# Performance work log

Hardware: AMD Instinct MI355X
Metric: run time of the kernel (lower is better)

Reference implementation:

```python
import jax, jax.numpy as jnp
import numpy as np

SIGMA = 0.248
PRNUM = 6
P = 7.5
K = 3.0
ALPHA = 2.5


def _gauss_kernel():
    # 5x5 normalized Gaussian, replicated per channel for depthwise conv [O=3,I=1,5,5]
    x = jnp.arange(-2, 3, dtype=jnp.float32)
    x2, y2 = jnp.meshgrid(x, x, indexing='xy')
    k = jnp.exp(-(x2 ** 2 + y2 ** 2) / (2.0 * SIGMA ** 2))
    k = k / jnp.sum(k)
    return jnp.broadcast_to(k[None, None], (3, 1, 5, 5))


def _dwconv(x, k):
    # x: [3,H,W]; depthwise 5x5 conv, padding=2 (matches F.conv2d(..., padding=2, groups=3))
    return jax.lax.conv_general_dilated(
        x[None], k, window_strides=(1, 1), padding=[(2, 2), (2, 2)],
        feature_group_count=3, dimension_numbers=('NCHW', 'OIHW', 'NCHW'))[0]


def _down2(x):
    # torch bilinear align_corners=False at exact scale 0.5 == 2x2 average pooling
    c, h, w = x.shape
    return x.reshape(c, h // 2, 2, w // 2, 2).mean(axis=(2, 4))


def _up(x, hw):
    # torch bilinear align_corners=False upsample (half-pixel centers) == jax linear resize
    return jax.image.resize(x, (x.shape[0], hw[0], hw[1]), method='linear')


def _foveate(img, fixs):
    C, H, W = img.shape
    k = _gauss_kernel()
    # build Gaussian pyramid
    G = img
    pyr = [G]
    for _ in range(1, PRNUM):
        G = _down2(_dwconv(G, k))
        pyr.append(G)
    # re-expand each level back to full res (interpolate then blur at each step)
    As = [pyr[0]]
    for i in range(1, PRNUM):
        cur = pyr[i]
        for j in range(i):
            hw = (cur.shape[1] * 2, cur.shape[2] * 2) if j < i - 1 else (H, W)
            cur = _dwconv(_up(cur, hw), k)
        As.append(cur)
    As = jnp.stack(As)  # [prNum, 3, H, W]

    # radial eccentricity map (min distance over fixations)
    x = jnp.arange(W, dtype=jnp.float32)
    y = jnp.arange(H, dtype=jnp.float32)
    x2d, y2d = jnp.meshgrid(x, y, indexing='xy')  # each [H, W]
    d = jnp.sqrt((x2d[None] - fixs[:, 0, None, None]) ** 2 +
                 (y2d[None] - fixs[:, 1, None, None]) ** 2) / P
    theta = jnp.min(d, axis=0)
    R = ALPHA / (theta + ALPHA)

    Ts = [jnp.exp(-((2.0 ** (i - 3)) * R / SIGMA) ** 2 * K) for i in range(1, PRNUM)]
    Ts.append(jnp.zeros_like(R))

    om = np.minimum(np.sqrt(np.log(2.0) / K) / (2.0 ** np.arange(-2, 3)) * SIGMA, 1.0)
    omega = np.concatenate([om, [0.0]]).astype(np.float32)  # [prNum]

    layer_ind = jnp.zeros_like(R)
    for i in range(1, PRNUM):
        ind = (R >= omega[i]) & (R <= omega[i - 1])
        layer_ind = jnp.where(ind, jnp.float32(i), layer_ind)

    Bs = [(0.5 - Ts[i]) / (Ts[i - 1] - Ts[i] + 1e-5) for i in range(1, PRNUM)]

    Ms = []
    for i in range(PRNUM):
        base = jnp.ones_like(R) if i == 0 else 1.0 - Bs[i - 1]
        M = jnp.where(layer_ind == i, base, jnp.float32(0.0))
        if i < PRNUM - 1:
            M = jnp.where(layer_ind == i + 1, Bs[i], M)
        Ms.append(M)
    Ms = jnp.stack(Ms)  # [prNum, H, W]

    # blend: sum_p Ms[p] * As[p, c]
    im_fov = jnp.einsum('phw,pchw->chw', Ms, As)
    return im_fov


def setup_inputs() -> dict:
    key = jax.random.key(0)
    k1, k2 = jax.random.split(key)
    img = jax.random.uniform(k1, (3, 2048, 2048), dtype=jnp.float32) * 255.0
    fixs = jax.random.uniform(k2, (4, 2), dtype=jnp.float32) * 2048.0
    return {'img': img, 'fixs': fixs}


def reference(img, fixs):
    return _foveate(img, fixs)
```

## Files before the change

### kernel.cpp

```cpp
#include <hip/hip_runtime.h>
#include <math.h>

#define HW2048 (2048ull*2048ull)
typedef float f4 __attribute__((ext_vector_type(4)));
typedef float f2 __attribute__((ext_vector_type(2)));
typedef _Float16 h8 __attribute__((ext_vector_type(8)));

struct BP {
  float P[4][3];
  float D2[5];
  float cc[5];
};

__global__ __launch_bounds__(256) void down12_k(const float* __restrict__ img,
                                                float* __restrict__ C1,
                                                float* __restrict__ p2) {
  int X = blockIdx.x * 16 + threadIdx.x;
  int Y = blockIdx.y * 16 + threadIdx.y;
  int c = blockIdx.z;
  const float* ip = img + (size_t)c * HW2048 + (size_t)(4 * Y) * 2048 + 4 * X;
  f4 r0 = __builtin_nontemporal_load((const f4*)(ip));
  f4 r1 = __builtin_nontemporal_load((const f4*)(ip + 2048));
  f4 r2 = __builtin_nontemporal_load((const f4*)(ip + 4096));
  f4 r3 = __builtin_nontemporal_load((const f4*)(ip + 6144));
  float a00 = 0.25f * (r0.x + r0.y + r1.x + r1.y);
  float a01 = 0.25f * (r0.z + r0.w + r1.z + r1.w);
  float a10 = 0.25f * (r2.x + r2.y + r3.x + r3.y);
  float a11 = 0.25f * (r2.z + r2.w + r3.z + r3.w);
  float* cp = C1 + (size_t)c * 1048576 + (size_t)(2 * Y) * 1024 + 2 * X;
  f2 u; u.x = a00; u.y = a01; *(f2*)cp = u;
  f2 v; v.x = a10; v.y = a11; *(f2*)(cp + 1024) = v;
  p2[((size_t)c * 512 + Y) * 512 + X] = 0.25f * (a00 + a01 + a10 + a11);
}

__global__ __launch_bounds__(256) void down345_k(const float* __restrict__ p2,
                                                 float* __restrict__ p3,
                                                 float* __restrict__ p4,
                                                 float* __restrict__ p5) {
  __shared__ float t4[16][17];
  int tx = threadIdx.x, ty = threadIdx.y;
  int X = blockIdx.x * 16 + tx;
  int Y = blockIdx.y * 16 + ty;
  int c = blockIdx.z;
  const float* ip = p2 + (size_t)c * 262144 + (size_t)(4 * Y) * 512 + 4 * X;
  f4 r0 = *(const f4*)(ip);
  f4 r1 = *(const f4*)(ip + 512);
  f4 r2 = *(const f4*)(ip + 1024);
  f4 r3 = *(const f4*)(ip + 1536);
  float a00 = 0.25f * (r0.x + r0.y + r1.x + r1.y);
  float a01 = 0.25f * (r0.z + r0.w + r1.z + r1.w);
  float a10 = 0.25f * (r2.x + r2.y + r3.x + r3.y);
  float a11 = 0.25f * (r2.z + r2.w + r3.z + r3.w);
  float* cp = p3 + (size_t)c * 65536 + (size_t)(2 * Y) * 256 + 2 * X;
  f2 u; u.x = a00; u.y = a01; *(f2*)cp = u;
  f2 v; v.x = a10; v.y = a11; *(f2*)(cp + 256) = v;
  float m = 0.25f * (a00 + a01 + a10 + a11);
  t4[ty][tx] = m;
  p4[((size_t)c * 128 + Y) * 128 + X] = m;
  __syncthreads();
  int tid = ty * 16 + tx;
  if (tid < 64) {
    int y = tid >> 3, x = tid & 7;
    float w = 0.25f * (t4[2*y][2*x] + t4[2*y][2*x+1] + t4[2*y+1][2*x] + t4[2*y+1][2*x+1]);
    p5[((size_t)c * 64 + blockIdx.y * 8 + y) * 64 + blockIdx.x * 8 + x] = w;
  }
}

__device__ __forceinline__ void up_coords(int o, int n, int& i0, int& i1, float& w0) {
  int m = o >> 1;
  if (o & 1) { i0 = m; i1 = min(m + 1, n - 1); w0 = 0.75f; }
  else       { i0 = max(m - 1, 0); i1 = m;     w0 = 0.25f; }
}

__global__ __launch_bounds__(256) void upchain_k(const float* __restrict__ p3,
                                                 const float* __restrict__ p4,
                                                 const float* __restrict__ p5,
                                                 float* __restrict__ U3,
                                                 float* __restrict__ U4,
                                                 float* __restrict__ U5) {
  __shared__ float a[19][20];
  __shared__ float mid[34][35];
  int z = blockIdx.z, im = z / 3, ch = z - im * 3;
  int X0 = blockIdx.x * 64, Y0 = blockIdx.y * 64;
  int tid = threadIdx.x;
  int bx1 = X0 / 4 - 1, by1 = Y0 / 4 - 1;
  int bx2 = X0 / 2 - 1, by2 = Y0 / 2 - 1;

  if (im == 2) {
    const float* s = p5 + ch * 4096;
    for (int j = tid; j < 18 * 18; j += 256) {
      int r = j / 18, cc = j % 18;
      int gy = min(max(by1 + r, 0), 127), gx = min(max(bx1 + cc, 0), 127);
      int r0, r1, c0, c1; float wy0, wx0;
      up_coords(gy, 64, r0, r1, wy0);
      up_coords(gx, 64, c0, c1, wx0);
      float wy1 = 1.f - wy0, wx1 = 1.f - wx0;
      a[r][cc] = wy0 * (wx0 * s[r0*64+c0] + wx1 * s[r0*64+c1])
               + wy1 * (wx0 * s[r1*64+c0] + wx1 * s[r1*64+c1]);
    }
    __syncthreads();
    for (int j = tid; j < 34 * 34; j += 256) {
      int r = j / 34, cc = j % 34;
      int gy = min(max(by2 + r, 0), 255), gx = min(max(bx2 + cc, 0), 255);
      int r0, r1, c0, c1; float wy0, wx0;
      up_coords(gy, 128, r0, r1, wy0);
      up_coords(gx, 128, c0, c1, wx0);
      float wy1 = 1.f - wy0, wx1 = 1.f - wx0;
      int a0 = r0 - by1, a1 = r1 - by1, b0 = c0 - bx1, b1 = c1 - bx1;
      mid[r][cc] = wy0 * (wx0 * a[a0][b0] + wx1 * a[a0][b1])
                 + wy1 * (wx0 * a[a1][b0] + wx1 * a[a1][b1]);
    }
    __syncthreads();
  } else if (im == 1) {
    const float* s = p4 + ch * 16384;
    for (int j = tid; j < 34 * 34; j += 256) {
      int r = j / 34, cc = j % 34;
      int gy = min(max(by2 + r, 0), 255), gx = min(max(bx2 + cc, 0), 255);
      int r0, r1, c0, c1; float wy0, wx0;
      up_coords(gy, 128, r0, r1, wy0);
      up_coords(gx, 128, c0, c1, wx0);
      float wy1 = 1.f - wy0, wx1 = 1.f - wx0;
      mid[r][cc] = wy0 * (wx0 * s[r0*128+c0] + wx1 * s[r0*128+c1])
                 + wy1 * (wx0 * s[r1*128+c0] + wx1 * s[r1*128+c1]);
    }
    __syncthreads();
  }

  float* dst = (im == 0) ? U3 : (im == 1) ? U4 : U5;
  const float* p3g = p3 + ch * 65536;
  int lx = tid & 63, lyb = tid >> 6;
#pragma unroll 4
  for (int rr = 0; rr < 16; ++rr) {
    int ly = lyb * 16 + rr;
    int x = X0 + lx, y = Y0 + ly;
    int r0, r1, c0, c1; float wy0, wx0;
    up_coords(y, 256, r0, r1, wy0);
    up_coords(x, 256, c0, c1, wx0);
    float wy1 = 1.f - wy0, wx1 = 1.f - wx0;
    float v;
    if (im == 0) {
      v = wy0 * (wx0 * p3g[r0*256+c0] + wx1 * p3g[r0*256+c1])
        + wy1 * (wx0 * p3g[r1*256+c0] + wx1 * p3g[r1*256+c1]);
    } else {
      int a0 = r0 - by2, a1 = r1 - by2, b0 = c0 - bx2, b1 = c1 - bx2;
      v = wy0 * (wx0 * mid[a0][b0] + wx1 * mid[a0][b1])
        + wy1 * (wx0 * mid[a1][b0] + wx1 * mid[a1][b1]);
    }
    dst[((size_t)ch * 512 + y) * 512 + x] = v;
  }
}

__device__ __forceinline__ float calc_B(float dd, int L, const BP& bp) {
  float d = sqrtf(dd);
  float R = 18.75f / (d + 18.75f);
  float R2 = R * R;
  float cL = (L == 1) ? bp.cc[1] : (L == 2) ? bp.cc[2] : (L == 3) ? bp.cc[3] : bp.cc[4];
  float cm = (L == 1) ? bp.cc[0] : (L == 2) ? bp.cc[1] : (L == 3) ? bp.cc[2] : (L == 4) ? bp.cc[3] : bp.cc[4];
  float tsL = (L >= 5) ? 0.f : __expf(-cL * R2);
  float tsm = __expf(-cm * R2);
  return (0.5f - tsL) / (tsm - tsL + 1e-5f);
}

__global__ __launch_bounds__(256) void classify_k(const float* __restrict__ fixs, int nf,
                                                  unsigned* __restrict__ meta,
                                                  h8* __restrict__ Bbuf, BP bp) {
  int xs = blockIdx.x * 64 + threadIdx.x;
  int yp = blockIdx.y * 4 + threadIdx.y;
  int x0 = xs * 4, y0 = yp * 2;
  int span = yp * 512 + xs;

  float d2[2][4];
#pragma unroll
  for (int j = 0; j < 2; ++j)
#pragma unroll
    for (int i = 0; i < 4; ++i) d2[j][i] = 3.4e38f;
  for (int f = 0; f < nf; ++f) {
    float dx0 = (float)x0 - fixs[2 * f], dy0 = (float)y0 - fixs[2 * f + 1];
#pragma unroll
    for (int j = 0; j < 2; ++j) {
      float dy = dy0 + (float)j, dy2 = dy * dy;
#pragma unroll
      for (int i = 0; i < 4; ++i) {
        float dx = dx0 + (float)i;
        d2[j][i] = fminf(d2[j][i], dx * dx + dy2);
      }
    }
  }

  unsigned m = 0;
  h8 b;
#pragma unroll
  for (int j = 0; j < 2; ++j)
#pragma unroll
    for (int i = 0; i < 4; ++i) {
      float dd = d2[j][i];
      int l = (dd >= bp.D2[0]) + (dd >= bp.D2[1]) + (dd >= bp.D2[2]) +
              (dd >= bp.D2[3]) + (dd >= bp.D2[4]);
      m |= (unsigned)l << (4 * (j * 4 + i));
      float B = (l == 0) ? 0.f : calc_B(dd, l, bp);
      b[j * 4 + i] = (_Float16)B;
    }
  meta[span] = m;
  Bbuf[span] = b;
}

__device__ __forceinline__ void phase_one(const BP& bp, int ph, float w[3]) {
#pragma unroll
  for (int t = 0; t < 3; ++t)
    w[t] = (ph == 0) ? bp.P[0][t] : (ph == 1) ? bp.P[1][t] : (ph == 2) ? bp.P[2][t] : bp.P[3][t];
}

__device__ __forceinline__ void s2c(const float* __restrict__ b, int x0, int y0,
                                    const BP& bp, float o[2][4]) {
  int t = x0 >> 2, ky = y0 >> 2, yph = y0 & 3;
  int c[3], r[3];
#pragma unroll
  for (int j = 0; j < 3; ++j) {
    c[j] = min(max(t - 1 + j, 0), 511);
    r[j] = min(max(ky - 1 + j, 0), 511);
  }
  float v[3][3];
#pragma unroll
  for (int j = 0; j < 3; ++j) {
    const float* row = b + r[j] * 512;
    v[j][0] = row[c[0]]; v[j][1] = row[c[1]]; v[j][2] = row[c[2]];
  }
  const float* wr0 = bp.P[yph];
  const float* wr1 = bp.P[yph + 1];
  float rv0[3], rv1[3];
#pragma unroll
  for (int i = 0; i < 3; ++i) {
    rv0[i] = wr0[0] * v[0][i] + wr0[1] * v[1][i] + wr0[2] * v[2][i];
    rv1[i] = wr1[0] * v[0][i] + wr1[1] * v[1][i] + wr1[2] * v[2][i];
  }
#pragma unroll
  for (int p = 0; p < 4; ++p) {
    o[0][p] = bp.P[p][0] * rv0[0] + bp.P[p][1] * rv0[1] + bp.P[p][2] * rv0[2];
    o[1][p] = bp.P[p][0] * rv1[0] + bp.P[p][1] * rv1[1] + bp.P[p][2] * rv1[2];
  }
}

__device__ __forceinline__ void s1c(const float* __restrict__ b, int x0, int y0,
                                    float o[2][4]) {
  int q0 = x0 >> 1, qy = y0 >> 1;
  int c[4], r[3];
#pragma unroll
  for (int i = 0; i < 4; ++i) c[i] = min(max(q0 - 1 + i, 0), 1023);
#pragma unroll
  for (int j = 0; j < 3; ++j) r[j] = min(max(qy - 1 + j, 0), 1023);
  float v[3][4];
#pragma unroll
  for (int j = 0; j < 3; ++j) {
    const float* row = b + r[j] * 1024;
    v[j][0] = row[c[0]]; v[j][1] = row[c[1]]; v[j][2] = row[c[2]]; v[j][3] = row[c[3]];
  }
  float rv0[4], rv1[4];
#pragma unroll
  for (int i = 0; i < 4; ++i) {
    rv0[i] = 0.25f * v[0][i] + 0.75f * v[1][i];
    rv1[i] = 0.75f * v[1][i] + 0.25f * v[2][i];
  }
  o[0][0] = 0.25f * rv0[0] + 0.75f * rv0[1];
  o[0][1] = 0.75f * rv0[1] + 0.25f * rv0[2];
  o[0][2] = 0.25f * rv0[1] + 0.75f * rv0[2];
  o[0][3] = 0.75f * rv0[2] + 0.25f * rv0[3];
  o[1][0] = 0.25f * rv1[0] + 0.75f * rv1[1];
  o[1][1] = 0.75f * rv1[1] + 0.25f * rv1[2];
  o[1][2] = 0.25f * rv1[1] + 0.75f * rv1[2];
  o[1][3] = 0.75f * rv1[2] + 0.25f * rv1[3];
}

__device__ float sample_pxc(int level, int x, int y,
                            const float* __restrict__ imgc, const float* __restrict__ C1c,
                            const float* __restrict__ b2, const float* __restrict__ b3,
                            const float* __restrict__ b4, const float* __restrict__ b5,
                            const BP& bp) {
  if (level == 0) return imgc[(size_t)y * 2048 + x];
  if (level == 1) {
    int r0, r1, c0, c1; float wy0, wx0;
    up_coords(y, 1024, r0, r1, wy0);
    up_coords(x, 1024, c0, c1, wx0);
    float wy1 = 1.f - wy0, wx1 = 1.f - wx0;
    return wy0 * (wx0 * C1c[r0 * 1024 + c0] + wx1 * C1c[r0 * 1024 + c1])
         + wy1 * (wx0 * C1c[r1 * 1024 + c0] + wx1 * C1c[r1 * 1024 + c1]);
  }
  const float* buf = (level == 2) ? b2 : (level == 3) ? b3 : (level == 4) ? b4 : b5;
  int ky = y >> 2, kx = x >> 2;
  float wr[3], wc[3];
  phase_one(bp, y & 3, wr);
  phase_one(bp, x & 3, wc);
  float acc = 0.f;
#pragma unroll
  for (int j = 0; j < 3; ++j) {
    int r = min(max(ky - 1 + j, 0), 511);
    const float* row = buf + r * 512;
    float cs = 0.f;
#pragma unroll
    for (int i = 0; i < 3; ++i) {
      int cidx = min(max(kx - 1 + i, 0), 511);
      cs += wc[i] * row[cidx];
    }
    acc += wr[j] * cs;
  }
  return acc;
}

__global__ __launch_bounds__(256) void blendc_k(
    const float* __restrict__ img, const float* __restrict__ C1,
    const float* __restrict__ B2, const float* __restrict__ B3,
    const float* __restrict__ B4, const float* __restrict__ B5,
    const unsigned* __restrict__ meta, const h8* __restrict__ Bbuf,
    float* __restrict__ out, BP bp) {
  int xs = blockIdx.x * 64 + threadIdx.x;
  int yp = blockIdx.y * 4 + threadIdx.y;
  int ch = blockIdx.z;
  int x0 = xs * 4, y0 = yp * 2;
  int span = yp * 512 + xs;
  size_t ob = (size_t)ch * HW2048 + (size_t)y0 * 2048 + x0;
  const float* imgc = img + (size_t)ch * HW2048;

  unsigned m = meta[span];

  if (m == 0u) {
    f4 v0 = *(const f4*)(imgc + (size_t)y0 * 2048 + x0);
    f4 v1 = *(const f4*)(imgc + (size_t)(y0 + 1) * 2048 + x0);
    __builtin_nontemporal_store(v0, (f4*)(out + ob));
    __builtin_nontemporal_store(v1, (f4*)(out + ob + 2048));
    return;
  }

  h8 bh = Bbuf[span];
  const float* C1c = C1 + (size_t)ch * 1048576;
  const float* b2 = B2 + (size_t)ch * 262144;
  const float* b3 = B3 + (size_t)ch * 262144;
  const float* b4 = B4 + (size_t)ch * 262144;
  const float* b5 = B5 + (size_t)ch * 262144;

  unsigned l0 = m & 15u;
  float res[2][4];

  if (m == l0 * 0x11111111u) {
    float hi[2][4], lo[2][4];
    if (l0 == 1) {
      s1c(C1c, x0, y0, hi);
      f4 v0 = *(const f4*)(imgc + (size_t)y0 * 2048 + x0);
      f4 v1 = *(const f4*)(imgc + (size_t)(y0 + 1) * 2048 + x0);
      lo[0][0] = v0.x; lo[0][1] = v0.y; lo[0][2] = v0.z; lo[0][3] = v0.w;
      lo[1][0] = v1.x; lo[1][1] = v1.y; lo[1][2] = v1.z; lo[1][3] = v1.w;
    } else {
      const float* hb = (l0 == 2) ? b2 : (l0 == 3) ? b3 : (l0 == 4) ? b4 : b5;
      s2c(hb, x0, y0, bp, hi);
      if (l0 == 2) s1c(C1c, x0, y0, lo);
      else {
        const float* lb = (l0 == 3) ? b2 : (l0 == 4) ? b3 : b4;
        s2c(lb, x0, y0, bp, lo);
      }
    }
#pragma unroll
    for (int j = 0; j < 2; ++j)
#pragma unroll
      for (int i = 0; i < 4; ++i) {
        float B = (float)bh[j * 4 + i];
        res[j][i] = B * lo[j][i] + (1.f - B) * hi[j][i];
      }
  } else {
#pragma unroll
    for (int j = 0; j < 2; ++j)
#pragma unroll
      for (int i = 0; i < 4; ++i) {
        int l = (int)((m >> (4 * (j * 4 + i))) & 15u);
        int px = x0 + i, py = y0 + j;
        if (l == 0) {
          res[j][i] = imgc[(size_t)py * 2048 + px];
        } else {
          float B = (float)bh[j * 4 + i];
          float hi = sample_pxc(l,     px, py, imgc, C1c, b2, b3, b4, b5, bp);
          float lo = sample_pxc(l - 1, px, py, imgc, C1c, b2, b3, b4, b5, bp);
          res[j][i] = B * lo + (1.f - B) * hi;
        }
      }
  }

  f4 v0, v1;
  v0.x = res[0][0]; v0.y = res[0][1]; v0.z = res[0][2]; v0.w = res[0][3];
  v1.x = res[1][0]; v1.y = res[1][1]; v1.z = res[1][2]; v1.w = res[1][3];
  __builtin_nontemporal_store(v0, (f4*)(out + ob));
  __builtin_nontemporal_store(v1, (f4*)(out + ob + 2048));
}

extern "C" void kernel_launch(void* const* d_in, const int* in_sizes, int n_in,
                              void* d_out, int out_size, void* d_ws, size_t ws_size,
                              hipStream_t stream) {
  const float* img  = (const float*)d_in[0];
  const float* fixs = (const float*)d_in[1];
  int nf = in_sizes[1] / 2;
  float* out = (float*)d_out;
  float* ws  = (float*)d_ws;

  BP bp;
  const double sig = 0.248, Kd = 3.0, Pd = 7.5, Ad = 2.5;
  double obv = sqrt(log(2.0) / Kd) * sig;
  for (int j = 0; j < 5; ++j) {
    double om = obv * pow(2.0, 2 - j);
    double Dj = Pd * Ad * (1.0 / om - 1.0);
    bp.D2[j] = (float)(Dj * Dj);
  }
  for (int X = 0; X < 5; ++X)
    bp.cc[X] = (float)(Kd * pow(2.0, 2.0 * (X - 2)) / (sig * sig));
  const float Pt[4][3] = {{0.375f, 0.625f, 0.f},
                          {0.1875f, 0.75f, 0.0625f},
                          {0.0625f, 0.75f, 0.1875f},
                          {0.f, 0.625f, 0.375f}};
  for (int a = 0; a < 4; ++a) for (int t = 0; t < 3; ++t) bp.P[a][t] = Pt[a][t];

  size_t o = 0;
  float* C1 = ws + o; o += 3ull * 1024 * 1024;
  float* p2 = ws + o; o += 3ull * 512 * 512;
  float* p3 = ws + o; o += 3ull * 256 * 256;
  float* p4 = ws + o; o += 3ull * 128 * 128;
  float* p5 = ws + o; o += 3ull * 64 * 64;
  float* U3 = ws + o; o += 3ull * 512 * 512;
  float* U4 = ws + o; o += 3ull * 512 * 512;
  float* U5 = ws + o; o += 3ull * 512 * 512;
  unsigned* meta = (unsigned*)(ws + o); o += 512ull * 1024;
  h8* Bbuf = (h8*)(ws + o); o += 4ull * 512 * 1024;

  down12_k  <<<dim3(32, 32, 3), dim3(16, 16), 0, stream>>>(img, C1, p2);
  down345_k <<<dim3(8, 8, 3),   dim3(16, 16), 0, stream>>>(p2, p3, p4, p5);
  upchain_k <<<dim3(8, 8, 9),   dim3(256),    0, stream>>>(p3, p4, p5, U3, U4, U5);
  classify_k<<<dim3(8, 256),    dim3(64, 4),  0, stream>>>(fixs, nf, meta, Bbuf, bp);
  blendc_k  <<<dim3(8, 256, 3), dim3(64, 4),  0, stream>>>(img, C1, p2, U3, U4, U5,
                                                           meta, Bbuf, out, bp);
}
```

Baseline: 158.4 us.

## Merge classify into upchain launch and blend 8x4 pixel tiles per thread

Measured after the change: 183.8 us. 16.0% more time.

```diff
diff --git a/kernel.cpp b/kernel.cpp
--- a/kernel.cpp
+++ b/kernel.cpp
@@ -72,15 +72,71 @@
   else       { i0 = max(m - 1, 0); i1 = m;     w0 = 0.25f; }
 }
 
-__global__ __launch_bounds__(256) void upchain_k(const float* __restrict__ p3,
+__device__ __forceinline__ float calc_B(float dd, int L, const BP& bp) {
+  float d = sqrtf(dd);
+  float R = 18.75f / (d + 18.75f);
+  float R2 = R * R;
+  float cL = (L == 1) ? bp.cc[1] : (L == 2) ? bp.cc[2] : (L == 3) ? bp.cc[3] : bp.cc[4];
+  float cm = (L == 1) ? bp.cc[0] : (L == 2) ? bp.cc[1] : (L == 3) ? bp.cc[2] : (L == 4) ? bp.cc[3] : bp.cc[4];
+  float tsL = (L >= 5) ? 0.f : __expf(-cL * R2);
+  float tsm = __expf(-cm * R2);
+  return (0.5f - tsL) / (tsm - tsL + 1e-5f);
+}
+
+__global__ __launch_bounds__(256) void upclass_k(const float* __restrict__ p3,
                                                  const float* __restrict__ p4,
                                                  const float* __restrict__ p5,
                                                  float* __restrict__ U3,
                                                  float* __restrict__ U4,
-                                                 float* __restrict__ U5) {
+                                                 float* __restrict__ U5,
+                                                 const float* __restrict__ fixs, int nf,
+                                                 unsigned* __restrict__ meta,
+                                                 h8* __restrict__ Bbuf, BP bp) {
   __shared__ float a[19][20];
   __shared__ float mid[34][35];
-  int z = blockIdx.z, im = z / 3, ch = z - im * 3;
+  int z = blockIdx.z;
+
+  if (z >= 9) {
+    int bid = (z - 9) * 64 + blockIdx.y * 8 + blockIdx.x;
+    int sid = bid * 256 + threadIdx.x;
+    int xs = sid & 511, yp = sid >> 9;
+    int x0 = xs * 4, y0 = yp * 2;
+    float d2[2][4];
+#pragma unroll
+    for (int j = 0; j < 2; ++j)
+#pragma unroll
+      for (int i = 0; i < 4; ++i) d2[j][i] = 3.4e38f;
+    for (int f = 0; f < nf; ++f) {
+      float dx0 = (float)x0 - fixs[2 * f], dy0 = (float)y0 - fixs[2 * f + 1];
+#pragma unroll
+      for (int j = 0; j < 2; ++j) {
+        float dy = dy0 + (float)j, dy2 = dy * dy;
+#pragma unroll
+        for (int i = 0; i < 4; ++i) {
+          float dx = dx0 + (float)i;
+          d2[j][i] = fminf(d2[j][i], dx * dx + dy2);
+        }
+      }
+    }
+    unsigned m = 0;
+    h8 b;
+#pragma unroll
+    for (int j = 0; j < 2; ++j)
+#pragma unroll
+      for (int i = 0; i < 4; ++i) {
+        float dd = d2[j][i];
+        int l = (dd >= bp.D2[0]) + (dd >= bp.D2[1]) + (dd >= bp.D2[2]) +
+                (dd >= bp.D2[3]) + (dd >= bp.D2[4]);
+        m |= (unsigned)l << (4 * (j * 4 + i));
+        float B = (l == 0) ? 0.f : calc_B(dd, l, bp);
+        b[j * 4 + i] = (_Float16)B;
+      }
+    meta[sid] = m;
+    Bbuf[sid] = b;
+    return;
+  }
+
+  int im = z / 3, ch = z - im * 3;
   int X0 = blockIdx.x * 64, Y0 = blockIdx.y * 64;
   int tid = threadIdx.x;
   int bx1 = X0 / 4 - 1, by1 = Y0 / 4 - 1;
@@ -150,64 +206,74 @@
   }
 }
 
-__device__ __forceinline__ float calc_B(float dd, int L, const BP& bp) {
-  float d = sqrtf(dd);
-  float R = 18.75f / (d + 18.75f);
-  float R2 = R * R;
-  float cL = (L == 1) ? bp.cc[1] : (L == 2) ? bp.cc[2] : (L == 3) ? bp.cc[3] : bp.cc[4];
-  float cm = (L == 1) ? bp.cc[0] : (L == 2) ? bp.cc[1] : (L == 3) ? bp.cc[2] : (L == 4) ? bp.cc[3] : bp.cc[4];
-  float tsL = (L >= 5) ? 0.f : __expf(-cL * R2);
-  float tsm = __expf(-cm * R2);
-  return (0.5f - tsL) / (tsm - tsL + 1e-5f);
-}
-
-__global__ __launch_bounds__(256) void classify_k(const float* __restrict__ fixs, int nf,
-                                                  unsigned* __restrict__ meta,
-                                                  h8* __restrict__ Bbuf, BP bp) {
-  int xs = blockIdx.x * 64 + threadIdx.x;
-  int yp = blockIdx.y * 4 + threadIdx.y;
-  int x0 = xs * 4, y0 = yp * 2;
-  int span = yp * 512 + xs;
-
-  float d2[2][4];
-#pragma unroll
-  for (int j = 0; j < 2; ++j)
-#pragma unroll
-    for (int i = 0; i < 4; ++i) d2[j][i] = 3.4e38f;
-  for (int f = 0; f < nf; ++f) {
-    float dx0 = (float)x0 - fixs[2 * f], dy0 = (float)y0 - fixs[2 * f + 1];
-#pragma unroll
-    for (int j = 0; j < 2; ++j) {
-      float dy = dy0 + (float)j, dy2 = dy * dy;
-#pragma unroll
-      for (int i = 0; i < 4; ++i) {
-        float dx = dx0 + (float)i;
-        d2[j][i] = fminf(d2[j][i], dx * dx + dy2);
-      }
-    }
-  }
-
-  unsigned m = 0;
-  h8 b;
-#pragma unroll
-  for (int j = 0; j < 2; ++j)
-#pragma unroll
-    for (int i = 0; i < 4; ++i) {
-      float dd = d2[j][i];
-      int l = (dd >= bp.D2[0]) + (dd >= bp.D2[1]) + (dd >= bp.D2[2]) +
-              (dd >= bp.D2[3]) + (dd >= bp.D2[4]);
-      m |= (unsigned)l << (4 * (j * 4 + i));
-      float B = (l == 0) ? 0.f : calc_B(dd, l, bp);
-      b[j * 4 + i] = (_Float16)B;
-    }
-  meta[span] = m;
-  Bbuf[span] = b;
-}
-
 __device__ __forceinline__ void phase_one(const BP& bp, int ph, float w[3]) {
 #pragma unroll
   for (int t = 0; t < 3; ++t)
     w[t] = (ph == 0) ? bp.P[0][t] : (ph == 1) ? bp.P[1][t] : (ph == 2) ? bp.P[2][t] : bp.P[3][t];
+}
+
+__device__ __forceinline__ void s2c8(const float* __restrict__ b, int x0, int y0,
+                                     const BP& bp, float o[4][8]) {
+  int t = x0 >> 2, ky = y0 >> 2;
+  int c[4], r[3];
+#pragma unroll
+  for (int i = 0; i < 4; ++i) c[i] = min(max(t - 1 + i, 0), 511);
+#pragma unroll
+  for (int j = 0; j < 3; ++j) r[j] = min(max(ky - 1 + j, 0), 511);
+  float v[3][4];
+#pragma unroll
+  for (int j = 0; j < 3; ++j) {
+    const float* row = b + r[j] * 512;
+    v[j][0] = row[c[0]]; v[j][1] = row[c[1]]; v[j][2] = row[c[2]]; v[j][3] = row[c[3]];
+  }
+  float rs[4][4];
+#pragma unroll
+  for (int ry = 0; ry < 4; ++ry)
+#pragma unroll
+    for (int i = 0; i < 4; ++i)
+      rs[ry][i] = bp.P[ry][0] * v[0][i] + bp.P[ry][1] * v[1][i] + bp.P[ry][2] * v[2][i];
+#pragma unroll
+  for (int ry = 0; ry < 4; ++ry) {
+#pragma unroll
+    for (int k = 0; k < 4; ++k)
+      o[ry][k] = bp.P[k][0] * rs[ry][0] + bp.P[k][1] * rs[ry][1] + bp.P[k][2] * rs[ry][2];
+#pragma unroll
+    for (int k = 0; k < 4; ++k)
+      o[ry][k + 4] = bp.P[k][0] * rs[ry][1] + bp.P[k][1] * rs[ry][2] + bp.P[k][2] * rs[ry][3];
+  }
+}
+
+__device__ __forceinline__ void s1c8(const float* __restrict__ b, int x0, int y0,
+                                     float o[4][8]) {
+  int q0 = x0 >> 1, qy = y0 >> 1;
+  int c[6], r[4];
+#pragma unroll
+  for (int i = 0; i < 6; ++i) c[i] = min(max(q0 - 1 + i, 0), 1023);
+#pragma unroll
+  for (int j = 0; j < 4; ++j) r[j] = min(max(qy - 1 + j, 0), 1023);
+  float v[4][6];
+#pragma unroll
+  for (int j = 0; j < 4; ++j) {
+    const float* row = b + r[j] * 1024;
+#pragma unroll
+    for (int i = 0; i < 6; ++i) v[j][i] = row[c[i]];
+  }
+  float rs[4][6];
+#pragma unroll
+  for (int i = 0; i < 6; ++i) {
+    rs[0][i] = 0.25f * v[0][i] + 0.75f * v[1][i];
+    rs[1][i] = 0.75f * v[1][i] + 0.25f * v[2][i];
+    rs[2][i] = 0.25f * v[1][i] + 0.75f * v[2][i];
+    rs[3][i] = 0.75f * v[2][i] + 0.25f * v[3][i];
+  }
+#pragma unroll
+  for (int ry = 0; ry < 4; ++ry)
+#pragma unroll
+    for (int k = 0; k < 8; ++k) {
+      int j = (k >> 1) + 1;
+      o[ry][k] = (k & 1) ? 0.75f * rs[ry][j] + 0.25f * rs[ry][j + 1]
+                         : 0.25f * rs[ry][j - 1] + 0.75f * rs[ry][j];
+    }
 }
 
 __device__ __forceinline__ void s2c(const float* __restrict__ b, int x0, int y0,
@@ -305,87 +371,151 @@
   return acc;
 }
 
-__global__ __launch_bounds__(256) void blendc_k(
+__global__ __launch_bounds__(256) void blendc8_k(
     const float* __restrict__ img, const float* __restrict__ C1,
     const float* __restrict__ B2, const float* __restrict__ B3,
     const float* __restrict__ B4, const float* __restrict__ B5,
     const unsigned* __restrict__ meta, const h8* __restrict__ Bbuf,
     float* __restrict__ out, BP bp) {
-  int xs = blockIdx.x * 64 + threadIdx.x;
-  int yp = blockIdx.y * 4 + threadIdx.y;
+  int xs8 = blockIdx.x * 64 + threadIdx.x;
+  int yq  = blockIdx.y * 4 + threadIdx.y;
   int ch = blockIdx.z;
-  int x0 = xs * 4, y0 = yp * 2;
-  int span = yp * 512 + xs;
+  int x0 = xs8 * 8, y0 = yq * 4;
+  int xsb = xs8 * 2, ypb = yq * 2;
+  unsigned m00 = meta[ypb * 512 + xsb],       m01 = meta[ypb * 512 + xsb + 1];
+  unsigned m10 = meta[(ypb + 1) * 512 + xsb], m11 = meta[(ypb + 1) * 512 + xsb + 1];
   size_t ob = (size_t)ch * HW2048 + (size_t)y0 * 2048 + x0;
   const float* imgc = img + (size_t)ch * HW2048;
 
-  unsigned m = meta[span];
-
-  if (m == 0u) {
-    f4 v0 = *(const f4*)(imgc + (size_t)y0 * 2048 + x0);
-    f4 v1 = *(const f4*)(imgc + (size_t)(y0 + 1) * 2048 + x0);
-    __builtin_nontemporal_store(v0, (f4*)(out + ob));
-    __builtin_nontemporal_store(v1, (f4*)(out + ob + 2048));
+  float res[4][8];
+
+  if ((m00 | m01 | m10 | m11) == 0u) {
+#pragma unroll
+    for (int ry = 0; ry < 4; ++ry) {
+      f4 a = *(const f4*)(imgc + (size_t)(y0 + ry) * 2048 + x0);
+      f4 b = *(const f4*)(imgc + (size_t)(y0 + ry) * 2048 + x0 + 4);
+      __builtin_nontemporal_store(a, (f4*)(out + ob + (size_t)ry * 2048));
+      __builtin_nontemporal_store(b, (f4*)(out + ob + (size_t)ry * 2048 + 4));
+    }
     return;
   }
 
-  h8 bh = Bbuf[span];
   const float* C1c = C1 + (size_t)ch * 1048576;
   const float* b2 = B2 + (size_t)ch * 262144;
   const float* b3 = B3 + (size_t)ch * 262144;
   const float* b4 = B4 + (size_t)ch * 262144;
   const float* b5 = B5 + (size_t)ch * 262144;
 
-  unsigned l0 = m & 15u;
-  float res[2][4];
-
-  if (m == l0 * 0x11111111u) {
-    float hi[2][4], lo[2][4];
+  unsigned l0 = m00 & 15u;
+  bool uni = (m00 == m01) && (m00 == m10) && (m00 == m11) && (m00 == l0 * 0x11111111u);
+
+  if (uni) {
+    h8 bh00 = Bbuf[ypb * 512 + xsb],       bh01 = Bbuf[ypb * 512 + xsb + 1];
+    h8 bh10 = Bbuf[(ypb + 1) * 512 + xsb], bh11 = Bbuf[(ypb + 1) * 512 + xsb + 1];
+    float hi[4][8], lo[4][8];
     if (l0 == 1) {
-      s1c(C1c, x0, y0, hi);
-      f4 v0 = *(const f4*)(imgc + (size_t)y0 * 2048 + x0);
-      f4 v1 = *(const f4*)(imgc + (size_t)(y0 + 1) * 2048 + x0);
-      lo[0][0] = v0.x; lo[0][1] = v0.y; lo[0][2] = v0.z; lo[0][3] = v0.w;
-      lo[1][0] = v1.x; lo[1][1] = v1.y; lo[1][2] = v1.z; lo[1][3] = v1.w;
+      s1c8(C1c, x0, y0, hi);
+#pragma unroll
+      for (int ry = 0; ry < 4; ++ry) {
+        f4 a = *(const f4*)(imgc + (size_t)(y0 + ry) * 2048 + x0);
+        f4 b = *(const f4*)(imgc + (size_t)(y0 + ry) * 2048 + x0 + 4);
+        lo[ry][0] = a.x; lo[ry][1] = a.y; lo[ry][2] = a.z; lo[ry][3] = a.w;
+        lo[ry][4] = b.x; lo[ry][5] = b.y; lo[ry][6] = b.z; lo[ry][7] = b.w;
+      }
+    } else if (l0 == 2) {
+      s2c8(b2, x0, y0, bp, hi);
+      s1c8(C1c, x0, y0, lo);
     } else {
-      const float* hb = (l0 == 2) ? b2 : (l0 == 3) ? b3 : (l0 == 4) ? b4 : b5;
-      s2c(hb, x0, y0, bp, hi);
-      if (l0 == 2) s1c(C1c, x0, y0, lo);
-      else {
-        const float* lb = (l0 == 3) ? b2 : (l0 == 4) ? b3 : b4;
-        s2c(lb, x0, y0, bp, lo);
-      }
-    }
-#pragma unroll
-    for (int j = 0; j < 2; ++j)
-#pragma unroll
-      for (int i = 0; i < 4; ++i) {
-        float B = (float)bh[j * 4 + i];
-        res[j][i] = B * lo[j][i] + (1.f - B) * hi[j][i];
+      const float* hb = (l0 == 3) ? b3 : (l0 == 4) ? b4 : b5;
+      const float* lb = (l0 == 3) ? b2 : (l0 == 4) ? b3 : b4;
+      s2c8(hb, x0, y0, bp, hi);
+      s2c8(lb, x0, y0, bp, lo);
+    }
+#pragma unroll
+    for (int ry = 0; ry < 4; ++ry)
+#pragma unroll
+      for (int k = 0; k < 8; ++k) {
+        int e = (ry & 1) * 4 + (k & 3);
+        float B = (float)((ry < 2) ? ((k < 4) ? bh00[e] : bh01[e])
+                                   : ((k < 4) ? bh10[e] : bh11[e]));
+        res[ry][k] = B * lo[ry][k] + (1.f - B) * hi[ry][k];
       }
   } else {
 #pragma unroll
-    for (int j = 0; j < 2; ++j)
-#pragma unroll
-      for (int i = 0; i < 4; ++i) {
-        int l = (int)((m >> (4 * (j * 4 + i))) & 15u);
-        int px = x0 + i, py = y0 + j;
-        if (l == 0) {
-          res[j][i] = imgc[(size_t)py * 2048 + px];
+    for (int sy = 0; sy < 2; ++sy)
+#pragma unroll
+      for (int sx = 0; sx < 2; ++sx) {
+        unsigned m = (sy == 0) ? ((sx == 0) ? m00 : m01) : ((sx == 0) ? m10 : m11);
+        int sx0 = x0 + sx * 4, sy0 = y0 + sy * 2;
+        float sub[2][4];
+        if (m == 0u) {
+#pragma unroll
+          for (int j = 0; j < 2; ++j) {
+            f4 v = *(const f4*)(imgc + (size_t)(sy0 + j) * 2048 + sx0);
+            sub[j][0] = v.x; sub[j][1] = v.y; sub[j][2] = v.z; sub[j][3] = v.w;
+          }
         } else {
-          float B = (float)bh[j * 4 + i];
-          float hi = sample_pxc(l,     px, py, imgc, C1c, b2, b3, b4, b5, bp);
-          float lo = sample_pxc(l - 1, px, py, imgc, C1c, b2, b3, b4, b5, bp);
-          res[j][i] = B * lo + (1.f - B) * hi;
+          h8 bh = Bbuf[(ypb + sy) * 512 + xsb + sx];
+          unsigned sl = m & 15u;
+          if (m == sl * 0x11111111u) {
+            float shi[2][4], slo[2][4];
+            if (sl == 1) {
+              s1c(C1c, sx0, sy0, shi);
+#pragma unroll
+              for (int j = 0; j < 2; ++j) {
+                f4 v = *(const f4*)(imgc + (size_t)(sy0 + j) * 2048 + sx0);
+                slo[j][0] = v.x; slo[j][1] = v.y; slo[j][2] = v.z; slo[j][3] = v.w;
+              }
+            } else {
+              const float* hb = (sl == 2) ? b2 : (sl == 3) ? b3 : (sl == 4) ? b4 : b5;
+              s2c(hb, sx0, sy0, bp, shi);
+              if (sl == 2) s1c(C1c, sx0, sy0, slo);
+              else {
+                const float* lb = (sl == 3) ? b2 : (sl == 4) ? b3 : b4;
+                s2c(lb, sx0, sy0, bp, slo);
+              }
+            }
+#pragma unroll
+            for (int j = 0; j < 2; ++j)
+#pragma unroll
+              for (int i = 0; i < 4; ++i) {
+                float B = (float)bh[j * 4 + i];
+                sub[j][i] = B * slo[j][i] + (1.f - B) * shi[j][i];
+              }
+          } else {
+#pragma unroll
+            for (int j = 0; j < 2; ++j)
+#pragma unroll
+              for (int i = 0; i < 4; ++i) {
+                int l = (int)((m >> (4 * (j * 4 + i))) & 15u);
+                int px = sx0 + i, py = sy0 + j;
+                if (l == 0) {
+                  sub[j][i] = imgc[(size_t)py * 2048 + px];
+                } else {
+                  float B = (float)bh[j * 4 + i];
+                  float hi = sample_pxc(l,     px, py, imgc, C1c, b2, b3, b4, b5, bp);
+                  float lo = sample_pxc(l - 1, px, py, imgc, C1c, b2, b3, b4, b5, bp);
+                  sub[j][i] = B * lo + (1.f - B) * hi;
+                }
+              }
+          }
         }
+#pragma unroll
+        for (int j = 0; j < 2; ++j)
+#pragma unroll
+          for (int i = 0; i < 4; ++i)
+            res[sy * 2 + j][sx * 4 + i] = sub[j][i];
       }
   }
 
-  f4 v0, v1;
-  v0.x = res[0][0]; v0.y = res[0][1]; v0.z = res[0][2]; v0.w = res[0][3];
-  v1.x = res[1][0]; v1.y = res[1][1]; v1.z = res[1][2]; v1.w = res[1][3];
-  __builtin_nontemporal_store(v0, (f4*)(out + ob));
-  __builtin_nontemporal_store(v1, (f4*)(out + ob + 2048));
+#pragma unroll
+  for (int ry = 0; ry < 4; ++ry) {
+    f4 a, b;
+    a.x = res[ry][0]; a.y = res[ry][1]; a.z = res[ry][2]; a.w = res[ry][3];
+    b.x = res[ry][4]; b.y = res[ry][5]; b.z = res[ry][6]; b.w = res[ry][7];
+    __builtin_nontemporal_store(a, (f4*)(out + ob + (size_t)ry * 2048));
+    __builtin_nontemporal_store(b, (f4*)(out + ob + (size_t)ry * 2048 + 4));
+  }
 }
 
 extern "C" void kernel_launch(void* const* d_in, const int* in_sizes, int n_in,
@@ -427,8 +557,8 @@
 
   down12_k  <<<dim3(32, 32, 3), dim3(16, 16), 0, stream>>>(img, C1, p2);
   down345_k <<<dim3(8, 8, 3),   dim3(16, 16), 0, stream>>>(p2, p3, p4, p5);
-  upchain_k <<<dim3(8, 8, 9),   dim3(256),    0, stream>>>(p3, p4, p5, U3, U4, U5);
-  classify_k<<<dim3(8, 256),    dim3(64, 4),  0, stream>>>(fixs, nf, meta, Bbuf, bp);
-  blendc_k  <<<dim3(8, 256, 3), dim3(64, 4),  0, stream>>>(img, C1, p2, U3, U4, U5,
+  upclass_k <<<dim3(8, 8, 41),  dim3(256),    0, stream>>>(p3, p4, p5, U3, U4, U5,
+                                                           fixs, nf, meta, Bbuf, bp);
+  blendc8_k <<<dim3(4, 128, 3), dim3(64, 4),  0, stream>>>(img, C1, p2, U3, U4, U5,
                                                            meta, Bbuf, out, bp);
 }
```

## Merge upchain and classify kernels, interleave adjacent pyramid levels into paired buffers

Applied to the files above, without the earlier changes.

After: 167.9 us. 6.0% more time.

```diff
diff --git a/kernel.cpp b/kernel.cpp
--- a/kernel.cpp
+++ b/kernel.cpp
@@ -72,62 +72,110 @@
   else       { i0 = max(m - 1, 0); i1 = m;     w0 = 0.25f; }
 }
 
-__global__ __launch_bounds__(256) void upchain_k(const float* __restrict__ p3,
+__device__ __forceinline__ float calc_B(float dd, int L, const BP& bp) {
+  float d = sqrtf(dd);
+  float R = 18.75f / (d + 18.75f);
+  float R2 = R * R;
+  float cL = (L == 1) ? bp.cc[1] : (L == 2) ? bp.cc[2] : (L == 3) ? bp.cc[3] : bp.cc[4];
+  float cm = (L == 1) ? bp.cc[0] : (L == 2) ? bp.cc[1] : (L == 3) ? bp.cc[2] : (L == 4) ? bp.cc[3] : bp.cc[4];
+  float tsL = (L >= 5) ? 0.f : __expf(-cL * R2);
+  float tsm = __expf(-cm * R2);
+  return (0.5f - tsL) / (tsm - tsL + 1e-5f);
+}
+
+__global__ __launch_bounds__(256) void upclass_k(const float* __restrict__ p2,
+                                                 const float* __restrict__ p3,
                                                  const float* __restrict__ p4,
                                                  const float* __restrict__ p5,
-                                                 float* __restrict__ U3,
-                                                 float* __restrict__ U4,
-                                                 float* __restrict__ U5) {
-  __shared__ float a[19][20];
-  __shared__ float mid[34][35];
-  int z = blockIdx.z, im = z / 3, ch = z - im * 3;
+                                                 f2* __restrict__ P23,
+                                                 f2* __restrict__ P34,
+                                                 f2* __restrict__ P45,
+                                                 const float* __restrict__ fixs, int nf,
+                                                 unsigned* __restrict__ meta,
+                                                 h8* __restrict__ Bbuf, BP bp) {
+  __shared__ float a[18][20];
+  __shared__ float m3[34][36];
+  __shared__ float m4[34][36];
+  __shared__ float m5[34][36];
+  int z = blockIdx.z;
+
+  if (z >= 3) {
+    int bid = (z - 3) * 64 + blockIdx.y * 8 + blockIdx.x;
+    int sid = bid * 256 + threadIdx.x;
+    int xs = sid & 511, yp = sid >> 9;
+    int x0 = xs * 4, y0 = yp * 2;
+    float d2[2][4];
+#pragma unroll
+    for (int j = 0; j < 2; ++j)
+#pragma unroll
+      for (int i = 0; i < 4; ++i) d2[j][i] = 3.4e38f;
+    for (int f = 0; f < nf; ++f) {
+      float dx0 = (float)x0 - fixs[2 * f], dy0 = (float)y0 - fixs[2 * f + 1];
+#pragma unroll
+      for (int j = 0; j < 2; ++j) {
+        float dy = dy0 + (float)j, dy2 = dy * dy;
+#pragma unroll
+        for (int i = 0; i < 4; ++i) {
+          float dx = dx0 + (float)i;
+          d2[j][i] = fminf(d2[j][i], dx * dx + dy2);
+        }
+      }
+    }
+    unsigned m = 0;
+    h8 b;
+#pragma unroll
+    for (int j = 0; j < 2; ++j)
+#pragma unroll
+      for (int i = 0; i < 4; ++i) {
+        float dd = d2[j][i];
+        int l = (dd >= bp.D2[0]) + (dd >= bp.D2[1]) + (dd >= bp.D2[2]) +
+                (dd >= bp.D2[3]) + (dd >= bp.D2[4]);
+        m |= (unsigned)l << (4 * (j * 4 + i));
+        float B = (l == 0) ? 0.f : calc_B(dd, l, bp);
+        b[j * 4 + i] = (_Float16)B;
+      }
+    meta[sid] = m;
+    Bbuf[sid] = b;
+    return;
+  }
+
+  int ch = z;
   int X0 = blockIdx.x * 64, Y0 = blockIdx.y * 64;
   int tid = threadIdx.x;
   int bx1 = X0 / 4 - 1, by1 = Y0 / 4 - 1;
   int bx2 = X0 / 2 - 1, by2 = Y0 / 2 - 1;
 
-  if (im == 2) {
-    const float* s = p5 + ch * 4096;
-    for (int j = tid; j < 18 * 18; j += 256) {
-      int r = j / 18, cc = j % 18;
-      int gy = min(max(by1 + r, 0), 127), gx = min(max(bx1 + cc, 0), 127);
-      int r0, r1, c0, c1; float wy0, wx0;
-      up_coords(gy, 64, r0, r1, wy0);
-      up_coords(gx, 64, c0, c1, wx0);
-      float wy1 = 1.f - wy0, wx1 = 1.f - wx0;
-      a[r][cc] = wy0 * (wx0 * s[r0*64+c0] + wx1 * s[r0*64+c1])
-               + wy1 * (wx0 * s[r1*64+c0] + wx1 * s[r1*64+c1]);
-    }
-    __syncthreads();
-    for (int j = tid; j < 34 * 34; j += 256) {
-      int r = j / 34, cc = j % 34;
-      int gy = min(max(by2 + r, 0), 255), gx = min(max(bx2 + cc, 0), 255);
-      int r0, r1, c0, c1; float wy0, wx0;
-      up_coords(gy, 128, r0, r1, wy0);
-      up_coords(gx, 128, c0, c1, wx0);
-      float wy1 = 1.f - wy0, wx1 = 1.f - wx0;
-      int a0 = r0 - by1, a1 = r1 - by1, b0 = c0 - bx1, b1 = c1 - bx1;
-      mid[r][cc] = wy0 * (wx0 * a[a0][b0] + wx1 * a[a0][b1])
-                 + wy1 * (wx0 * a[a1][b0] + wx1 * a[a1][b1]);
-    }
-    __syncthreads();
-  } else if (im == 1) {
-    const float* s = p4 + ch * 16384;
-    for (int j = tid; j < 34 * 34; j += 256) {
-      int r = j / 34, cc = j % 34;
-      int gy = min(max(by2 + r, 0), 255), gx = min(max(bx2 + cc, 0), 255);
-      int r0, r1, c0, c1; float wy0, wx0;
-      up_coords(gy, 128, r0, r1, wy0);
-      up_coords(gx, 128, c0, c1, wx0);
-      float wy1 = 1.f - wy0, wx1 = 1.f - wx0;
-      mid[r][cc] = wy0 * (wx0 * s[r0*128+c0] + wx1 * s[r0*128+c1])
-                 + wy1 * (wx0 * s[r1*128+c0] + wx1 * s[r1*128+c1]);
-    }
-    __syncthreads();
-  }
-
-  float* dst = (im == 0) ? U3 : (im == 1) ? U4 : U5;
-  const float* p3g = p3 + ch * 65536;
+  const float* s5 = p5 + ch * 4096;
+  for (int j = tid; j < 18 * 18; j += 256) {
+    int r = j / 18, cc = j - r * 18;
+    int gy = min(max(by1 + r, 0), 127), gx = min(max(bx1 + cc, 0), 127);
+    int r0, r1, c0, c1; float wy0, wx0;
+    up_coords(gy, 64, r0, r1, wy0);
+    up_coords(gx, 64, c0, c1, wx0);
+    float wy1 = 1.f - wy0, wx1 = 1.f - wx0;
+    a[r][cc] = wy0 * (wx0 * s5[r0*64+c0] + wx1 * s5[r0*64+c1])
+             + wy1 * (wx0 * s5[r1*64+c0] + wx1 * s5[r1*64+c1]);
+  }
+  __syncthreads();
+  const float* s4 = p4 + ch * 16384;
+  const float* s3 = p3 + ch * 65536;
+  for (int j = tid; j < 34 * 34; j += 256) {
+    int r = j / 34, cc = j - r * 34;
+    int gy = min(max(by2 + r, 0), 255), gx = min(max(bx2 + cc, 0), 255);
+    int r0, r1, c0, c1; float wy0, wx0;
+    up_coords(gy, 128, r0, r1, wy0);
+    up_coords(gx, 128, c0, c1, wx0);
+    float wy1 = 1.f - wy0, wx1 = 1.f - wx0;
+    int a0 = r0 - by1, a1 = r1 - by1, b0 = c0 - bx1, b1 = c1 - bx1;
+    m5[r][cc] = wy0 * (wx0 * a[a0][b0] + wx1 * a[a0][b1])
+              + wy1 * (wx0 * a[a1][b0] + wx1 * a[a1][b1]);
+    m4[r][cc] = wy0 * (wx0 * s4[r0*128+c0] + wx1 * s4[r0*128+c1])
+              + wy1 * (wx0 * s4[r1*128+c0] + wx1 * s4[r1*128+c1]);
+    m3[r][cc] = s3[gy * 256 + gx];
+  }
+  __syncthreads();
+
+  const float* p2g = p2 + ch * 262144;
   int lx = tid & 63, lyb = tid >> 6;
 #pragma unroll 4
   for (int rr = 0; rr < 16; ++rr) {
@@ -137,71 +185,20 @@
     up_coords(y, 256, r0, r1, wy0);
     up_coords(x, 256, c0, c1, wx0);
     float wy1 = 1.f - wy0, wx1 = 1.f - wx0;
-    float v;
-    if (im == 0) {
-      v = wy0 * (wx0 * p3g[r0*256+c0] + wx1 * p3g[r0*256+c1])
-        + wy1 * (wx0 * p3g[r1*256+c0] + wx1 * p3g[r1*256+c1]);
-    } else {
-      int a0 = r0 - by2, a1 = r1 - by2, b0 = c0 - bx2, b1 = c1 - bx2;
-      v = wy0 * (wx0 * mid[a0][b0] + wx1 * mid[a0][b1])
-        + wy1 * (wx0 * mid[a1][b0] + wx1 * mid[a1][b1]);
-    }
-    dst[((size_t)ch * 512 + y) * 512 + x] = v;
-  }
-}
-
-__device__ __forceinline__ float calc_B(float dd, int L, const BP& bp) {
-  float d = sqrtf(dd);
-  float R = 18.75f / (d + 18.75f);
-  float R2 = R * R;
-  float cL = (L == 1) ? bp.cc[1] : (L == 2) ? bp.cc[2] : (L == 3) ? bp.cc[3] : bp.cc[4];
-  float cm = (L == 1) ? bp.cc[0] : (L == 2) ? bp.cc[1] : (L == 3) ? bp.cc[2] : (L == 4) ? bp.cc[3] : bp.cc[4];
-  float tsL = (L >= 5) ? 0.f : __expf(-cL * R2);
-  float tsm = __expf(-cm * R2);
-  return (0.5f - tsL) / (tsm - tsL + 1e-5f);
-}
-
-__global__ __launch_bounds__(256) void classify_k(const float* __restrict__ fixs, int nf,
-                                                  unsigned* __restrict__ meta,
-                                                  h8* __restrict__ Bbuf, BP bp) {
-  int xs = blockIdx.x * 64 + threadIdx.x;
-  int yp = blockIdx.y * 4 + threadIdx.y;
-  int x0 = xs * 4, y0 = yp * 2;
-  int span = yp * 512 + xs;
-
-  float d2[2][4];
-#pragma unroll
-  for (int j = 0; j < 2; ++j)
-#pragma unroll
-    for (int i = 0; i < 4; ++i) d2[j][i] = 3.4e38f;
-  for (int f = 0; f < nf; ++f) {
-    float dx0 = (float)x0 - fixs[2 * f], dy0 = (float)y0 - fixs[2 * f + 1];
-#pragma unroll
-    for (int j = 0; j < 2; ++j) {
-      float dy = dy0 + (float)j, dy2 = dy * dy;
-#pragma unroll
-      for (int i = 0; i < 4; ++i) {
-        float dx = dx0 + (float)i;
-        d2[j][i] = fminf(d2[j][i], dx * dx + dy2);
-      }
-    }
-  }
-
-  unsigned m = 0;
-  h8 b;
-#pragma unroll
-  for (int j = 0; j < 2; ++j)
-#pragma unroll
-    for (int i = 0; i < 4; ++i) {
-      float dd = d2[j][i];
-      int l = (dd >= bp.D2[0]) + (dd >= bp.D2[1]) + (dd >= bp.D2[2]) +
-              (dd >= bp.D2[3]) + (dd >= bp.D2[4]);
-      m |= (unsigned)l << (4 * (j * 4 + i));
-      float B = (l == 0) ? 0.f : calc_B(dd, l, bp);
-      b[j * 4 + i] = (_Float16)B;
-    }
-  meta[span] = m;
-  Bbuf[span] = b;
+    int a0 = r0 - by2, a1 = r1 - by2, b0 = c0 - bx2, b1 = c1 - bx2;
+    float u3 = wy0 * (wx0 * m3[a0][b0] + wx1 * m3[a0][b1])
+             + wy1 * (wx0 * m3[a1][b0] + wx1 * m3[a1][b1]);
+    float u4 = wy0 * (wx0 * m4[a0][b0] + wx1 * m4[a0][b1])
+             + wy1 * (wx0 * m4[a1][b0] + wx1 * m4[a1][b1]);
+    float u5 = wy0 * (wx0 * m5[a0][b0] + wx1 * m5[a0][b1])
+             + wy1 * (wx0 * m5[a1][b0] + wx1 * m5[a1][b1]);
+    float p2v = p2g[(size_t)y * 512 + x];
+    size_t idx = ((size_t)ch * 512 + y) * 512 + x;
+    f2 w;
+    w.x = p2v; w.y = u3; P23[idx] = w;
+    w.x = u3;  w.y = u4; P34[idx] = w;
+    w.x = u4;  w.y = u5; P45[idx] = w;
+  }
 }
 
 __device__ __forceinline__ void phase_one(const BP& bp, int ph, float w[3]) {
@@ -210,8 +207,8 @@
     w[t] = (ph == 0) ? bp.P[0][t] : (ph == 1) ? bp.P[1][t] : (ph == 2) ? bp.P[2][t] : bp.P[3][t];
 }
 
-__device__ __forceinline__ void s2c(const float* __restrict__ b, int x0, int y0,
-                                    const BP& bp, float o[2][4]) {
+__device__ __forceinline__ void s2p(const f2* __restrict__ pb, int x0, int y0,
+                                    const BP& bp, float cx[2][4], float cy[2][4]) {
   int t = x0 >> 2, ky = y0 >> 2, yph = y0 & 3;
   int c[3], r[3];
 #pragma unroll
@@ -219,15 +216,15 @@
     c[j] = min(max(t - 1 + j, 0), 511);
     r[j] = min(max(ky - 1 + j, 0), 511);
   }
-  float v[3][3];
+  f2 v[3][3];
 #pragma unroll
   for (int j = 0; j < 3; ++j) {
-    const float* row = b + r[j] * 512;
+    const f2* row = pb + (size_t)r[j] * 512;
     v[j][0] = row[c[0]]; v[j][1] = row[c[1]]; v[j][2] = row[c[2]];
   }
   const float* wr0 = bp.P[yph];
   const float* wr1 = bp.P[yph + 1];
-  float rv0[3], rv1[3];
+  f2 rv0[3], rv1[3];
 #pragma unroll
   for (int i = 0; i < 3; ++i) {
     rv0[i] = wr0[0] * v[0][i] + wr0[1] * v[1][i] + wr0[2] * v[2][i];
@@ -235,8 +232,10 @@
   }
 #pragma unroll
   for (int p = 0; p < 4; ++p) {
-    o[0][p] = bp.P[p][0] * rv0[0] + bp.P[p][1] * rv0[1] + bp.P[p][2] * rv0[2];
-    o[1][p] = bp.P[p][0] * rv1[0] + bp.P[p][1] * rv1[1] + bp.P[p][2] * rv1[2];
+    f2 a0 = bp.P[p][0] * rv0[0] + bp.P[p][1] * rv0[1] + bp.P[p][2] * rv0[2];
+    f2 a1 = bp.P[p][0] * rv1[0] + bp.P[p][1] * rv1[1] + bp.P[p][2] * rv1[2];
+    cx[0][p] = a0.x; cy[0][p] = a0.y;
+    cx[1][p] = a1.x; cy[1][p] = a1.y;
   }
 }
 
@@ -251,7 +250,7 @@
   float v[3][4];
 #pragma unroll
   for (int j = 0; j < 3; ++j) {
-    const float* row = b + r[j] * 1024;
+    const float* row = b + (size_t)r[j] * 1024;
     v[j][0] = row[c[0]]; v[j][1] = row[c[1]]; v[j][2] = row[c[2]]; v[j][3] = row[c[3]];
   }
   float rv0[4], rv1[4];
@@ -270,45 +269,40 @@
   o[1][3] = 0.75f * rv1[2] + 0.25f * rv1[3];
 }
 
-__device__ float sample_pxc(int level, int x, int y,
-                            const float* __restrict__ imgc, const float* __restrict__ C1c,
-                            const float* __restrict__ b2, const float* __restrict__ b3,
-                            const float* __restrict__ b4, const float* __restrict__ b5,
-                            const BP& bp) {
-  if (level == 0) return imgc[(size_t)y * 2048 + x];
-  if (level == 1) {
-    int r0, r1, c0, c1; float wy0, wx0;
-    up_coords(y, 1024, r0, r1, wy0);
-    up_coords(x, 1024, c0, c1, wx0);
-    float wy1 = 1.f - wy0, wx1 = 1.f - wx0;
-    return wy0 * (wx0 * C1c[r0 * 1024 + c0] + wx1 * C1c[r0 * 1024 + c1])
-         + wy1 * (wx0 * C1c[r1 * 1024 + c0] + wx1 * C1c[r1 * 1024 + c1]);
-  }
-  const float* buf = (level == 2) ? b2 : (level == 3) ? b3 : (level == 4) ? b4 : b5;
+__device__ __forceinline__ f2 spx_pair(const f2* __restrict__ pb, int x, int y,
+                                       const BP& bp) {
   int ky = y >> 2, kx = x >> 2;
   float wr[3], wc[3];
   phase_one(bp, y & 3, wr);
   phase_one(bp, x & 3, wc);
-  float acc = 0.f;
+  f2 acc; acc.x = 0.f; acc.y = 0.f;
 #pragma unroll
   for (int j = 0; j < 3; ++j) {
     int r = min(max(ky - 1 + j, 0), 511);
-    const float* row = buf + r * 512;
-    float cs = 0.f;
+    const f2* row = pb + (size_t)r * 512;
+    f2 cs; cs.x = 0.f; cs.y = 0.f;
 #pragma unroll
     for (int i = 0; i < 3; ++i) {
-      int cidx = min(max(kx - 1 + i, 0), 511);
-      cs += wc[i] * row[cidx];
+      int ci = min(max(kx - 1 + i, 0), 511);
+      cs += wc[i] * row[ci];
     }
     acc += wr[j] * cs;
   }
   return acc;
 }
 
+__device__ __forceinline__ float s1px(const float* __restrict__ C1c, int x, int y) {
+  int r0, r1, c0, c1; float wy0, wx0;
+  up_coords(y, 1024, r0, r1, wy0);
+  up_coords(x, 1024, c0, c1, wx0);
+  float wy1 = 1.f - wy0, wx1 = 1.f - wx0;
+  return wy0 * (wx0 * C1c[(size_t)r0 * 1024 + c0] + wx1 * C1c[(size_t)r0 * 1024 + c1])
+       + wy1 * (wx0 * C1c[(size_t)r1 * 1024 + c0] + wx1 * C1c[(size_t)r1 * 1024 + c1]);
+}
+
 __global__ __launch_bounds__(256) void blendc_k(
     const float* __restrict__ img, const float* __restrict__ C1,
-    const float* __restrict__ B2, const float* __restrict__ B3,
-    const float* __restrict__ B4, const float* __restrict__ B5,
+    const f2* __restrict__ P23, const f2* __restrict__ P34, const f2* __restrict__ P45,
     const unsigned* __restrict__ meta, const h8* __restrict__ Bbuf,
     float* __restrict__ out, BP bp) {
   int xs = blockIdx.x * 64 + threadIdx.x;
@@ -320,40 +314,45 @@
   const float* imgc = img + (size_t)ch * HW2048;
 
   unsigned m = meta[span];
-
-  if (m == 0u) {
+  unsigned l0 = m & 15u;
+  const f2* P23c = P23 + (size_t)ch * 262144;
+  const f2* P34c = P34 + (size_t)ch * 262144;
+  const f2* P45c = P45 + (size_t)ch * 262144;
+  const float* C1c = C1 + (size_t)ch * 1048576;
+
+  float res[2][4];
+
+  if (m == l0 * 0x11111111u && l0 >= 3u) {
+    const f2* pb = (l0 == 3) ? P23c : (l0 == 4) ? P34c : P45c;
+    float lo[2][4], hi[2][4];
+    s2p(pb, x0, y0, bp, lo, hi);
+    h8 bh = Bbuf[span];
+#pragma unroll
+    for (int j = 0; j < 2; ++j)
+#pragma unroll
+      for (int i = 0; i < 4; ++i) {
+        float B = (float)bh[j * 4 + i];
+        res[j][i] = B * lo[j][i] + (1.f - B) * hi[j][i];
+      }
+  } else if (m == 0u) {
     f4 v0 = *(const f4*)(imgc + (size_t)y0 * 2048 + x0);
     f4 v1 = *(const f4*)(imgc + (size_t)(y0 + 1) * 2048 + x0);
     __builtin_nontemporal_store(v0, (f4*)(out + ob));
     __builtin_nontemporal_store(v1, (f4*)(out + ob + 2048));
     return;
-  }
-
-  h8 bh = Bbuf[span];
-  const float* C1c = C1 + (size_t)ch * 1048576;
-  const float* b2 = B2 + (size_t)ch * 262144;
-  const float* b3 = B3 + (size_t)ch * 262144;
-  const float* b4 = B4 + (size_t)ch * 262144;
-  const float* b5 = B5 + (size_t)ch * 262144;
-
-  unsigned l0 = m & 15u;
-  float res[2][4];
-
-  if (m == l0 * 0x11111111u) {
+  } else if (m == l0 * 0x11111111u) {
+    h8 bh = Bbuf[span];
     float hi[2][4], lo[2][4];
-    if (l0 == 1) {
+    if (l0 == 2) {
+      float dummy[2][4];
+      s2p(P23c, x0, y0, bp, hi, dummy);
+      s1c(C1c, x0, y0, lo);
+    } else {
       s1c(C1c, x0, y0, hi);
-      f4 v0 = *(const f4*)(imgc + (size_t)y0 * 2048 + x0);
-      f4 v1 = *(const f4*)(imgc + (size_t)(y0 + 1) * 2048 + x0);
-      lo[0][0] = v0.x; lo[0][1] = v0.y; lo[0][2] = v0.z; lo[0][3] = v0.w;
-      lo[1][0] = v1.x; lo[1][1] = v1.y; lo[1][2] = v1.z; lo[1][3] = v1.w;
-    } else {
-      const float* hb = (l0 == 2) ? b2 : (l0 == 3) ? b3 : (l0 == 4) ? b4 : b5;
-      s2c(hb, x0, y0, bp, hi);
-      if (l0 == 2) s1c(C1c, x0, y0, lo);
-      else {
-        const float* lb = (l0 == 3) ? b2 : (l0 == 4) ? b3 : b4;
-        s2c(lb, x0, y0, bp, lo);
+#pragma unroll
+      for (int j = 0; j < 2; ++j) {
+        f4 v = *(const f4*)(imgc + (size_t)(y0 + j) * 2048 + x0);
+        lo[j][0] = v.x; lo[j][1] = v.y; lo[j][2] = v.z; lo[j][3] = v.w;
       }
     }
 #pragma unroll
@@ -364,6 +363,7 @@
         res[j][i] = B * lo[j][i] + (1.f - B) * hi[j][i];
       }
   } else {
+    h8 bh = Bbuf[span];
 #pragma unroll
     for (int j = 0; j < 2; ++j)
 #pragma unroll
@@ -374,8 +374,19 @@
           res[j][i] = imgc[(size_t)py * 2048 + px];
         } else {
           float B = (float)bh[j * 4 + i];
-          float hi = sample_pxc(l,     px, py, imgc, C1c, b2, b3, b4, b5, bp);
-          float lo = sample_pxc(l - 1, px, py, imgc, C1c, b2, b3, b4, b5, bp);
+          float lo, hi;
+          if (l >= 3) {
+            const f2* pb = (l == 3) ? P23c : (l == 4) ? P34c : P45c;
+            f2 g = spx_pair(pb, px, py, bp);
+            lo = g.x; hi = g.y;
+          } else if (l == 2) {
+            f2 g = spx_pair(P23c, px, py, bp);
+            hi = g.x;
+            lo = s1px(C1c, px, py);
+          } else {
+            hi = s1px(C1c, px, py);
+            lo = imgc[(size_t)py * 2048 + px];
+          }
           res[j][i] = B * lo + (1.f - B) * hi;
         }
       }
@@ -419,16 +430,17 @@
   float* p3 = ws + o; o += 3ull * 256 * 256;
   float* p4 = ws + o; o += 3ull * 128 * 128;
   float* p5 = ws + o; o += 3ull * 64 * 64;
-  float* U3 = ws + o; o += 3ull * 512 * 512;
-  float* U4 = ws + o; o += 3ull * 512 * 512;
-  float* U5 = ws + o; o += 3ull * 512 * 512;
+  f2* P23 = (f2*)(ws + o); o += 2ull * 3 * 512 * 512;
+  f2* P34 = (f2*)(ws + o); o += 2ull * 3 * 512 * 512;
+  f2* P45 = (f2*)(ws + o); o += 2ull * 3 * 512 * 512;
   unsigned* meta = (unsigned*)(ws + o); o += 512ull * 1024;
   h8* Bbuf = (h8*)(ws + o); o += 4ull * 512 * 1024;
 
   down12_k  <<<dim3(32, 32, 3), dim3(16, 16), 0, stream>>>(img, C1, p2);
   down345_k <<<dim3(8, 8, 3),   dim3(16, 16), 0, stream>>>(p2, p3, p4, p5);
-  upchain_k <<<dim3(8, 8, 9),   dim3(256),    0, stream>>>(p3, p4, p5, U3, U4, U5);
-  classify_k<<<dim3(8, 256),    dim3(64, 4),  0, stream>>>(fixs, nf, meta, Bbuf, bp);
-  blendc_k  <<<dim3(8, 256, 3), dim3(64, 4),  0, stream>>>(img, C1, p2, U3, U4, U5,
+  upclass_k <<<dim3(8, 8, 35),  dim3(256),    0, stream>>>(p2, p3, p4, p5,
+                                                           P23, P34, P45,
+                                                           fixs, nf, meta, Bbuf, bp);
+  blendc_k  <<<dim3(8, 256, 3), dim3(64, 4),  0, stream>>>(img, C1, P23, P34, P45,
                                                            meta, Bbuf, out, bp);
 }
```
